# Kernel optimization log

Hardware: AMD Instinct MI355X
Metric: run time of the kernel (lower is better)

Reference implementation:

```python
import jax, jax.numpy as jnp
import numpy as np

N_NODES = 50000
NUM_FEA = 213
HID, IN_HEAD = 16, 12
OUT_DIM, OUT_HEAD = 8, 8
NEG_SLOPE = 0.2


def gat_conv(x, W, att_src, att_dst, bias, src, dst, H, C):
    # x: [N, F] -> h: [N, H, C]
    N = x.shape[0]
    h = (x @ W).reshape(N, H, C)
    a_s = jnp.sum(h * att_src, axis=-1)  # [N, H]
    a_d = jnp.sum(h * att_dst, axis=-1)  # [N, H]
    e = jax.nn.leaky_relu(a_s[src] + a_d[dst], NEG_SLOPE)  # [E, H]
    # segment softmax over incoming edges of each dst node
    m = jax.ops.segment_max(e, dst, num_segments=N)
    ex = jnp.exp(e - m[dst])
    denom = jax.ops.segment_sum(ex, dst, num_segments=N)
    alpha = ex / denom[dst]  # [E, H]
    out = jax.ops.segment_sum(h[src] * alpha[:, :, None], dst, num_segments=N)
    return out.reshape(N, H * C) + bias


def setup_inputs() -> dict:
    key = jax.random.key(0)
    ks = jax.random.split(key, 16)
    E = 800000
    P = 16384
    features = jax.random.normal(ks[0], (N_NODES, NUM_FEA), dtype=jnp.float32)
    edge_index = jax.random.randint(ks[1], (2, E), 0, N_NODES, dtype=jnp.int32)
    node1_index = jax.random.randint(ks[2], (P,), 0, N_NODES, dtype=jnp.int32)
    node2_index = jax.random.randint(ks[3], (P,), 0, N_NODES, dtype=jnp.int32)
    s1 = 1.0 / np.sqrt(NUM_FEA)
    s2 = 1.0 / np.sqrt(HID * IN_HEAD)
    s3 = 1.0 / np.sqrt(OUT_DIM * OUT_HEAD * 2)
    params = {
        'W1': jax.random.normal(ks[4], (NUM_FEA, IN_HEAD * HID), jnp.float32) * s1,
        'att_src1': jax.random.normal(ks[5], (IN_HEAD, HID), jnp.float32) * s1,
        'att_dst1': jax.random.normal(ks[6], (IN_HEAD, HID), jnp.float32) * s1,
        'b1': jnp.zeros((IN_HEAD * HID,), jnp.float32),
        'W2': jax.random.normal(ks[7], (IN_HEAD * HID, OUT_HEAD * OUT_DIM), jnp.float32) * s2,
        'att_src2': jax.random.normal(ks[8], (OUT_HEAD, OUT_DIM), jnp.float32) * s2,
        'att_dst2': jax.random.normal(ks[9], (OUT_HEAD, OUT_DIM), jnp.float32) * s2,
        'b2': jnp.zeros((OUT_HEAD * OUT_DIM,), jnp.float32),
        'linW': jax.random.normal(ks[10], (OUT_DIM * OUT_HEAD * 2, 2), jnp.float32) * s3,
        'linb': jnp.zeros((2,), jnp.float32),
    }
    return dict(features=features, edge_index=edge_index,
                node1_index=node1_index, node2_index=node2_index, **params)


def reference(features, edge_index, node1_index, node2_index,
              W1, att_src1, att_dst1, b1, W2, att_src2, att_dst2, b2, linW, linb):
    # eval mode: dropout(p=0.8) is identity
    N = features.shape[0]
    self_loops = jnp.arange(N, dtype=edge_index.dtype)
    src = jnp.concatenate([edge_index[0], self_loops])
    dst = jnp.concatenate([edge_index[1], self_loops])
    x = gat_conv(features, W1, att_src1, att_dst1, b1, src, dst, IN_HEAD, HID)
    x = jax.nn.elu(x)
    x = gat_conv(x, W2, att_src2, att_dst2, b2, src, dst, OUT_HEAD, OUT_DIM)
    x = jax.nn.elu(x)
    pair = jnp.concatenate([x[node1_index], x[node2_index]], axis=1)
    y_pred = jax.nn.sigmoid(pair @ linW + linb)
    return (y_pred, x)
```

## Files before the change

kernel.cpp:

```cpp
#include <hip/hip_runtime.h>
#include <hip/hip_bf16.h>

#define HID1 16
#define NHEAD1 12
#define F1 (HID1*NHEAD1)
#define HID2 8
#define NHEAD2 8
#define F2 (HID2*NHEAD2)
#define NUM_FEA 213
#define NEG_SLOPE 0.2f
#define KP 224
#define KP2 192
#define LDK 40
#define MR1 64
#define MR2 64
#define NC1 224
#define NW2R 80
#define SLOTS 56
#define BINS 256
#define NPB 196
#define CAP 4096
#define FILLB 256
#define EPT 13

typedef __attribute__((ext_vector_type(8))) __bf16 bf16x8;
typedef __attribute__((ext_vector_type(4))) float floatx4;
typedef __attribute__((ext_vector_type(2))) float floatx2;
typedef float floatx4u __attribute__((ext_vector_type(4), aligned(4)));
typedef unsigned short ushort_t;

static __device__ __forceinline__ unsigned short f2bf(float f) {
    unsigned u = __float_as_uint(f);
    unsigned r = (u + 0x7fffu + ((u >> 16) & 1u)) >> 16;
    return (unsigned short)r;
}
static __device__ __forceinline__ float lrelu(float e) {
    return e > 0.f ? e : NEG_SLOPE * e;
}
static __device__ __forceinline__ float elu(float v) {
    return v > 0.f ? v : (__expf(v) - 1.f);
}


__global__ __launch_bounds__(256) void prep_kernel(
        const float* __restrict__ W1, const float* __restrict__ as1w,
        const float* __restrict__ ad1w, ushort_t* __restrict__ Wt1,
        const float* __restrict__ W2, const float* __restrict__ as2w,
        const float* __restrict__ ad2w, ushort_t* __restrict__ Wt2,
        const int* __restrict__ ei, int* __restrict__ binctr,
        unsigned* __restrict__ binbuf, int E, int Etot, int nwb) {
    int b = (int)blockIdx.x;
    int tid = threadIdx.x;
    if (b >= nwb) {
        __shared__ int hist[BINS];
        __shared__ int cur[BINS];
        int fb = b - nwb;
        if (tid < BINS) hist[tid] = 0;
        __syncthreads();
        unsigned stash[EPT];
        int base_e = fb * 256 + tid;
#pragma unroll
        for (int i = 0; i < EPT; i++) {
            int e = base_e + i * (FILLB * 256);
            unsigned pk = 0xffffffffu;
            if (e < Etot) {
                int s, d;
                if (e < E) { s = ei[e]; d = ei[E + e]; } else { s = e - E; d = s; }
                pk = (unsigned)s | ((unsigned)d << 16);
                atomicAdd(&hist[(unsigned)d / NPB], 1);
            }
            stash[i] = pk;
        }
        __syncthreads();
        if (tid < BINS) cur[tid] = atomicAdd(&binctr[tid], hist[tid]);
        __syncthreads();
#pragma unroll
        for (int i = 0; i < EPT; i++) {
            unsigned pk = stash[i];
            if (pk != 0xffffffffu) {
                int d = (int)(pk >> 16);
                int bin = (int)((unsigned)d / NPB);
                int dl = d - bin * NPB;
                int r = atomicAdd(&cur[bin], 1);
                if (r < CAP)
                    binbuf[(long)bin * CAP + r] = (pk & 0xffffu) | ((unsigned)dl << 16);
            }
        }
        return;
    }
    int j = b * 256 + tid;
    if (j < NC1 * KP) {
        int n = j / KP, k = j - n * KP;
        float v = 0.f;
        if (k < NUM_FEA) {
            if (n < 192) {
                v = W1[(long)k * F1 + n];
            } else if (n < 204) {
                int hd = n - 192;
                for (int c = 0; c < HID1; c++)
                    v += W1[(long)k * F1 + hd * HID1 + c] * as1w[hd * HID1 + c];
            } else if (n < 216) {
                int hd = n - 204;
                for (int c = 0; c < HID1; c++)
                    v += W1[(long)k * F1 + hd * HID1 + c] * ad1w[hd * HID1 + c];
            }
        }
        Wt1[j] = f2bf(v);
    } else {
        int j2 = j - NC1 * KP;
        if (j2 < NW2R * KP2) {
            int n = j2 / KP2, k = j2 - n * KP2;
            float v;
            if (n < 64) {
                v = W2[(long)k * F2 + n];
            } else if (n < 72) {
                int hd = n - 64;
                v = 0.f;
                for (int c = 0; c < HID2; c++)
                    v += W2[(long)k * F2 + hd * HID2 + c] * as2w[hd * HID2 + c];
            } else {
                int hd = n - 72;
                v = 0.f;
                for (int c = 0; c < HID2; c++)
                    v += W2[(long)k * F2 + hd * HID2 + c] * ad2w[hd * HID2 + c];
            }
            Wt2[j2] = f2bf(v);
        }
    }
}


static __device__ __forceinline__ void stageA(ushort_t* dst, const float* xp,
                                              bool ok, int col) {
    union { int4 q; ushort_t u[8]; } pk;
    if (ok && col + 8 <= NUM_FEA) {
        floatx4u a = *(const floatx4u*)(xp + col);
        floatx4u c = *(const floatx4u*)(xp + col + 4);
#pragma unroll
        for (int j = 0; j < 4; j++) { pk.u[j] = f2bf(a[j]); pk.u[4 + j] = f2bf(c[j]); }
    } else {
#pragma unroll
        for (int j = 0; j < 8; j++) {
            float v = (ok && col + j < NUM_FEA) ? xp[col + j] : 0.f;
            pk.u[j] = f2bf(v);
        }
    }
    *(int4*)dst = pk.q;
}

__global__ __launch_bounds__(256) void gemm1_bs_kernel(
        const float* __restrict__ X, const ushort_t* __restrict__ Wt,
        ushort_t* __restrict__ Hout, float* __restrict__ as_, float* __restrict__ ad_,
        const unsigned* __restrict__ binbuf, const int* __restrict__ binctr,
        ushort_t* __restrict__ esrcp, int* __restrict__ cnt,
        int N, int nblk_gemm) {
    __shared__ ushort_t As[MR1 * LDK];
    __shared__ ushort_t Bs[NC1 * LDK];
    __shared__ int lcnt[NPB];
    int tid = threadIdx.x;
    if ((int)blockIdx.x >= nblk_gemm) {
        int b = (int)blockIdx.x - nblk_gemm;
        if (tid < NPB) lcnt[tid] = 0;
        __syncthreads();
        int cntb = binctr[b];
        if (cntb > CAP) cntb = CAP;
        const unsigned* seg = binbuf + (long)b * CAP;
        for (int t = tid; t < cntb; t += 256) {
            unsigned u = seg[t];
            int s = (int)(u & 0xffffu);
            int dl = (int)(u >> 16);
            int slot = atomicAdd(&lcnt[dl], 1);
            if (slot < SLOTS)
                esrcp[(long)(b * NPB + dl) * SLOTS + slot] = (ushort_t)s;
        }
        __syncthreads();
        int d = b * NPB + tid;
        if (tid < NPB && d < N) cnt[d] = lcnt[tid];
        return;
    }
    int wave = tid >> 6, lane = tid & 63;
    int q = lane >> 4, l16 = lane & 15;
    int wm = (wave >> 1) * 32;
    int wn = (wave & 1) * 112;
    long row0 = (long)blockIdx.x * MR1;

    int r0 = tid >> 2, ksl = (tid & 3) * 8;
    long gr0 = row0 + r0;
    bool ok0 = gr0 < N;
    const float* xp0 = X + gr0 * NUM_FEA;
    ushort_t* lds0 = &As[r0 * LDK + ksl];

    floatx4 acc[2][7] = {};

    for (int k0 = 0; k0 < KP; k0 += 32) {
        stageA(lds0, xp0, ok0, k0 + ksl);
#pragma unroll
        for (int p = 0; p < 4; p++) {
            int idx = p * 256 + tid;
            if (idx < NC1 * 4) {
                int r = idx >> 2, ks = (idx & 3) * 8;
                *(int4*)&Bs[r * LDK + ks] = *(const int4*)&Wt[(long)r * KP + k0 + ks];
            }
        }
        __syncthreads();
        bf16x8 af[2], bfr[7];
#pragma unroll
        for (int rt = 0; rt < 2; rt++)
            af[rt] = *(const bf16x8*)&As[(wm + rt * 16 + l16) * LDK + q * 8];
#pragma unroll
        for (int ct = 0; ct < 7; ct++)
            bfr[ct] = *(const bf16x8*)&Bs[(wn + ct * 16 + l16) * LDK + q * 8];
#pragma unroll
        for (int rt = 0; rt < 2; rt++)
#pragma unroll
            for (int ct = 0; ct < 7; ct++)
                acc[rt][ct] = __builtin_amdgcn_mfma_f32_16x16x32_bf16(af[rt], bfr[ct], acc[rt][ct], 0, 0, 0);
        __syncthreads();
    }
#pragma unroll
    for (int rt = 0; rt < 2; rt++) {
#pragma unroll
        for (int r = 0; r < 4; r++) {
            long grow = row0 + wm + rt * 16 + q * 4 + r;
            if (grow < N) {
#pragma unroll
                for (int ct = 0; ct < 7; ct++) {
                    int col = wn + ct * 16 + l16;
                    float v = acc[rt][ct][r];
                    if (col < 192)      Hout[grow * F1 + col] = f2bf(v);
                    else if (col < 204) as_[grow * NHEAD1 + col - 192] = v;
                    else if (col < 216) ad_[grow * NHEAD1 + col - 204] = v;
                }
            }
        }
    }
}


__global__ __launch_bounds__(256) void gemm2_mfma(const ushort_t* __restrict__ Xbf,
                                                  const ushort_t* __restrict__ Wt,
                                                  ushort_t* __restrict__ Hout,
                                                  float* __restrict__ as_,
                                                  float* __restrict__ ad_, int N) {
    __shared__ ushort_t As[MR2 * LDK];
    __shared__ ushort_t Bs[96 * LDK];
    int tid = threadIdx.x;
    int wave = tid >> 6, lane = tid & 63;
    int q = lane >> 4, l16 = lane & 15;
    int wm = (wave >> 1) * 32;
    int wn = (wave & 1) * 48;
    long row0 = (long)blockIdx.x * MR2;

    int r0 = tid >> 2, ksl = (tid & 3) * 8;

    floatx4 acc[2][3] = {};

    for (int k0 = 0; k0 < KP2; k0 += 32) {
        *(int4*)&As[r0 * LDK + ksl] = *(const int4*)&Xbf[(row0 + r0) * KP2 + k0 + ksl];
#pragma unroll
        for (int p = 0; p < 2; p++) {
            int idx = p * 256 + tid;
            if (idx < 96 * 4) {
                int r = idx >> 2, ks = (idx & 3) * 8;
                int4 z = {0, 0, 0, 0};
                *(int4*)&Bs[r * LDK + ks] = (r < NW2R) ? *(const int4*)&Wt[(long)r * KP2 + k0 + ks] : z;
            }
        }
        __syncthreads();
        bf16x8 af[2], bfr[3];
#pragma unroll
        for (int rt = 0; rt < 2; rt++)
            af[rt] = *(const bf16x8*)&As[(wm + rt * 16 + l16) * LDK + q * 8];
#pragma unroll
        for (int ct = 0; ct < 3; ct++)
            bfr[ct] = *(const bf16x8*)&Bs[(wn + ct * 16 + l16) * LDK + q * 8];
#pragma unroll
        for (int rt = 0; rt < 2; rt++)
#pragma unroll
            for (int ct = 0; ct < 3; ct++)
                acc[rt][ct] = __builtin_amdgcn_mfma_f32_16x16x32_bf16(af[rt], bfr[ct], acc[rt][ct], 0, 0, 0);
        __syncthreads();
    }
#pragma unroll
    for (int rt = 0; rt < 2; rt++) {
#pragma unroll
        for (int r = 0; r < 4; r++) {
            long grow = row0 + wm + rt * 16 + q * 4 + r;
            if (grow < N) {
#pragma unroll
                for (int ct = 0; ct < 3; ct++) {
                    int col = wn + ct * 16 + l16;
                    float v = acc[rt][ct][r];
                    if (col < 64)      Hout[grow * F2 + col] = f2bf(v);
                    else if (col < 72) as_[grow * NHEAD2 + col - 64] = v;
                    else if (col < 80) ad_[grow * NHEAD2 + col - 72] = v;
                }
            }
        }
    }
}


__global__ __launch_bounds__(256) void gather1_kernel(const int* __restrict__ cnt,
                                                      const ushort_t* __restrict__ esrcp,
                                                      const float* __restrict__ as_,
                                                      const float* __restrict__ ad_,
                                                      const ushort_t* __restrict__ h,
                                                      const float* __restrict__ bias,
                                                      ushort_t* __restrict__ xout, int N) {
    int d = blockIdx.x * 4 + (threadIdx.x >> 6);
    if (d >= N) return;
    int l = threadIdx.x & 63;
    int jc = l < 48 ? l : 47;
    int hj = jc >> 2;
    int e0 = l / 12, h0 = l - e0 * 12;
    int l64 = l + 64;
    int e1 = l64 / 12, h1 = l64 - e1 * 12;
    int deg = cnt[d]; if (deg > SLOTS) deg = SLOTS;
    int sfull = (int)esrcp[d * SLOTS + (l < SLOTS - 1 ? l : SLOTS - 1)];
    float adv0 = ad_[d * NHEAD1 + h0];
    float adv1 = ad_[d * NHEAD1 + h1];
    float4 b4 = ((const float4*)bias)[jc];
    const char* hcol = (const char*)(h + 4 * jc);

    floatx2 a01 = {0.f, 0.f}, a23 = {0.f, 0.f};
    float accd = 0.f;

    for (int p0 = 0; p0 < deg; p0 += 8) {
        int s_e[8];
#pragma unroll
        for (int i = 0; i < 8; i++) s_e[i] = __shfl(sfull, p0 + i, 64);
        uint2 g[8];
#pragma unroll
        for (int i = 0; i < 8; i++) {
            unsigned off = (unsigned)s_e[i] * (unsigned)(F1 * 2);
            g[i] = *(const uint2*)(hcol + off);
        }
        int sq0 = __shfl(sfull, p0 + e0, 64);
        int sq1 = __shfl(sfull, p0 + e1, 64);
        float a0v = as_[sq0 * NHEAD1 + h0];
        float a1v = as_[sq1 * NHEAD1 + h1];
        float w0 = (p0 + e0 < deg) ? __expf(lrelu(a0v + adv0)) : 0.f;
        float w1 = (e1 < 8 && p0 + e1 < deg) ? __expf(lrelu(a1v + adv1)) : 0.f;
#pragma unroll
        for (int i = 0; i < 8; i++) {
            float wi;
            if (i <= 4) {
                wi = __shfl(w0, i * 12 + hj, 64);
            } else if (i == 5) {
                float wa = __shfl(w0, 60 + hj, 64);
                int srcb = hj >= 4 ? hj - 4 : 0;
                float wb = __shfl(w1, srcb, 64);
                wi = (hj < 4) ? wa : wb;
            } else {
                wi = __shfl(w1, i * 12 + hj - 64, 64);
            }
            unsigned x = g[i].x, y = g[i].y;
            floatx2 h01, h23, w2;
            h01.x = __uint_as_float(x << 16);
            h01.y = __uint_as_float(x & 0xffff0000u);
            h23.x = __uint_as_float(y << 16);
            h23.y = __uint_as_float(y & 0xffff0000u);
            w2.x = wi; w2.y = wi;
            a01 += w2 * h01;
            a23 += w2 * h23;
            accd += wi;
        }
    }
    if (l < 48) {
        float inv = __builtin_amdgcn_rcpf(accd);
        float v0 = elu(a01.x * inv + b4.x);
        float v1 = elu(a01.y * inv + b4.y);
        float v2 = elu(a23.x * inv + b4.z);
        float v3 = elu(a23.y * inv + b4.w);
        uint2 outp;
        outp.x = (unsigned)f2bf(v0) | ((unsigned)f2bf(v1) << 16);
        outp.y = (unsigned)f2bf(v2) | ((unsigned)f2bf(v3) << 16);
        *(uint2*)(xout + (long)d * F1 + 4 * l) = outp;
    }
}


__global__ __launch_bounds__(256) void gather2_kernel(const int* __restrict__ cnt,
                                                      const ushort_t* __restrict__ esrcp,
                                                      const float* __restrict__ as_,
                                                      const float* __restrict__ ad_,
                                                      const ushort_t* __restrict__ h,
                                                      const float* __restrict__ bias,
                                                      float* __restrict__ xout, int N) {
    int d = blockIdx.x * 4 + (threadIdx.x >> 6);
    if (d >= N) return;
    int l = threadIdx.x & 63;
    int cg = l & 15;
    int hj = cg >> 1;
    int e_lo = l >> 4;
    int ie0 = l >> 3, hq = l & 7;
    int ie1 = 8 + ie0;
    int deg = cnt[d]; if (deg > SLOTS) deg = SLOTS;
    int sfull = (int)esrcp[d * SLOTS + (l < SLOTS - 1 ? l : SLOTS - 1)];
    float advq = ad_[d * NHEAD2 + hq];
    const char* hcol = (const char*)(h + 4 * cg);

    floatx2 a01 = {0.f, 0.f}, a23 = {0.f, 0.f};
    float accd = 0.f;

    for (int p0 = 0; p0 < deg; p0 += 16) {
        int se[4];
#pragma unroll
        for (int k = 0; k < 4; k++) se[k] = __shfl(sfull, p0 + e_lo + 4 * k, 64);
        uint2 g[4];
#pragma unroll
        for (int k = 0; k < 4; k++) {
            unsigned off = (unsigned)se[k] * (unsigned)(F2 * 2);
            g[k] = *(const uint2*)(hcol + off);
        }
        int sq0 = __shfl(sfull, p0 + ie0, 64);
        int sq1 = __shfl(sfull, p0 + ie1, 64);
        float a0v = as_[sq0 * NHEAD2 + hq];
        float a1v = as_[sq1 * NHEAD2 + hq];
        float w0d = (p0 + ie0 < deg) ? __expf(lrelu(a0v + advq)) : 0.f;
        float w1d = (p0 + ie1 < deg) ? __expf(lrelu(a1v + advq)) : 0.f;
#pragma unroll
        for (int k = 0; k < 4; k++) {
            int i = e_lo + 4 * k;
            float wk = (k < 2) ? __shfl(w0d, i * 8 + hj, 64)
                               : __shfl(w1d, i * 8 + hj - 64, 64);
            unsigned x = g[k].x, y = g[k].y;
            floatx2 h01, h23, w2;
            h01.x = __uint_as_float(x << 16);
            h01.y = __uint_as_float(x & 0xffff0000u);
            h23.x = __uint_as_float(y << 16);
            h23.y = __uint_as_float(y & 0xffff0000u);
            w2.x = wk; w2.y = wk;
            a01 += w2 * h01;
            a23 += w2 * h23;
            accd += wk;
        }
    }
    a01.x += __shfl_xor(a01.x, 16, 64); a01.x += __shfl_xor(a01.x, 32, 64);
    a01.y += __shfl_xor(a01.y, 16, 64); a01.y += __shfl_xor(a01.y, 32, 64);
    a23.x += __shfl_xor(a23.x, 16, 64); a23.x += __shfl_xor(a23.x, 32, 64);
    a23.y += __shfl_xor(a23.y, 16, 64); a23.y += __shfl_xor(a23.y, 32, 64);
    accd  += __shfl_xor(accd, 16, 64);  accd  += __shfl_xor(accd, 32, 64);
    if (l < 16) {
        float4 b4 = ((const float4*)bias)[cg];
        float inv = __builtin_amdgcn_rcpf(accd);
        float4 outp;
        outp.x = elu(a01.x * inv + b4.x);
        outp.y = elu(a01.y * inv + b4.y);
        outp.z = elu(a23.x * inv + b4.z);
        outp.w = elu(a23.y * inv + b4.w);
        *(float4*)(xout + (long)d * F2 + 4 * cg) = outp;
    }
}


__global__ void pair_kernel(const float* __restrict__ x, const int* __restrict__ n1,
                            const int* __restrict__ n2, const float* __restrict__ linW,
                            const float* __restrict__ linb, float* __restrict__ y, int P) {
    int idx = blockIdx.x * blockDim.x + threadIdx.x;
    if (idx >= P) return;
    const float4* xa = (const float4*)(x + (long)n1[idx] * F2);
    const float4* xb = (const float4*)(x + (long)n2[idx] * F2);
    float a0 = linb[0], a1 = linb[1];
#pragma unroll
    for (int k4 = 0; k4 < F2 / 4; k4++) {
        float4 v = xa[k4];
        int k = k4 * 4;
        a0 += v.x * linW[2 * k] + v.y * linW[2 * (k + 1)] + v.z * linW[2 * (k + 2)] + v.w * linW[2 * (k + 3)];
        a1 += v.x * linW[2 * k + 1] + v.y * linW[2 * (k + 1) + 1] + v.z * linW[2 * (k + 2) + 1] + v.w * linW[2 * (k + 3) + 1];
    }
#pragma unroll
    for (int k4 = 0; k4 < F2 / 4; k4++) {
        float4 v = xb[k4];
        int k = F2 + k4 * 4;
        a0 += v.x * linW[2 * k] + v.y * linW[2 * (k + 1)] + v.z * linW[2 * (k + 2)] + v.w * linW[2 * (k + 3)];
        a1 += v.x * linW[2 * k + 1] + v.y * linW[2 * (k + 1) + 1] + v.z * linW[2 * (k + 2) + 1] + v.w * linW[2 * (k + 3) + 1];
    }
    y[2 * idx]     = 1.f / (1.f + __expf(-a0));
    y[2 * idx + 1] = 1.f / (1.f + __expf(-a1));
}


extern "C" void kernel_launch(void* const* d_in, const int* in_sizes, int n_in,
                              void* d_out, int out_size, void* d_ws, size_t ws_size,
                              hipStream_t stream) {
    const float* features = (const float*)d_in[0];
    const int*   ei       = (const int*)d_in[1];
    const int*   n1       = (const int*)d_in[2];
    const int*   n2       = (const int*)d_in[3];
    const float* W1       = (const float*)d_in[4];
    const float* att_s1   = (const float*)d_in[5];
    const float* att_d1   = (const float*)d_in[6];
    const float* b1       = (const float*)d_in[7];
    const float* W2       = (const float*)d_in[8];
    const float* att_s2   = (const float*)d_in[9];
    const float* att_d2   = (const float*)d_in[10];
    const float* b2       = (const float*)d_in[11];
    const float* linW     = (const float*)d_in[12];
    const float* linb     = (const float*)d_in[13];

    const int N = in_sizes[0] / NUM_FEA;
    const int E = in_sizes[1] / 2;
    const int P = in_sizes[2];
    const int Etot = E + N;

    const int nblk1 = (N + MR1 - 1) / MR1;
    const int nblk2 = (N + MR2 - 1) / MR2;
    const int nwb = (NC1 * KP + NW2R * KP2 + 255) / 256;

    float* ws = (float*)d_ws;
    long o = 0;
    float* h1r  = ws + o; o += (long)N * F1 / 2;
    float* x1r  = ws + o; o += (long)N * F1 / 2;
    float* as1  = ws + o; o += (long)N * NHEAD1;
    float* ad1  = ws + o; o += (long)N * NHEAD1;
    float* h2r  = ws + o; o += (long)N * F2 / 2;
    float* as2  = ws + o; o += (long)N * NHEAD2;
    float* ad2  = ws + o; o += (long)N * NHEAD2;
    float* w1r  = ws + o; o += ((long)NC1 * KP + 1) / 2;
    float* w2r  = ws + o; o += ((long)NW2R * KP2 + 1) / 2;
    float* esr  = ws + o; o += ((long)N * SLOTS + 1) / 2;
    unsigned* binbuf = (unsigned*)(ws + o); o += (long)BINS * CAP;
    int* binctr = (int*)(ws + o); o += BINS;
    int* cnt  = (int*)(ws + o); o += N;

    ushort_t* h1b   = (ushort_t*)h1r;
    ushort_t* x1bf  = (ushort_t*)x1r;
    ushort_t* h2b   = (ushort_t*)h2r;
    ushort_t* Wt1   = (ushort_t*)w1r;
    ushort_t* Wt2   = (ushort_t*)w2r;
    ushort_t* esrcp = (ushort_t*)esr;

    float* y_out = (float*)d_out;
    float* x_out = (float*)d_out + (long)2 * P;

    hipMemsetAsync(binctr, 0, (size_t)BINS * sizeof(int), stream);

    prep_kernel<<<nwb + FILLB, 256, 0, stream>>>(
        W1, att_s1, att_d1, Wt1, W2, att_s2, att_d2, Wt2,
        ei, binctr, binbuf, E, Etot, nwb);

    gemm1_bs_kernel<<<nblk1 + BINS, 256, 0, stream>>>(
        features, Wt1, h1b, as1, ad1, binbuf, binctr, esrcp, cnt, N, nblk1);

    gather1_kernel<<<(N + 3) / 4, 256, 0, stream>>>(cnt, esrcp, as1, ad1, h1b, b1, x1bf, N);

    gemm2_mfma<<<nblk2, 256, 0, stream>>>(x1bf, Wt2, h2b, as2, ad2, N);
    gather2_kernel<<<(N + 3) / 4, 256, 0, stream>>>(cnt, esrcp, as2, ad2, h2b, b2, x_out, N);

    pair_kernel<<<(P + 255) / 256, 256, 0, stream>>>(x_out, n1, n2, linW, linb, y_out, P);
}
```

Measured before the change: 252.0 us.

## Move edge binning fill into GEMM1 launch and split bin sort into own kernel

The edge binning fill stage moves out of the weight-prep kernel and runs as extra blocks alongside the GEMM1 blocks. The per-bin local sort, which previously shared the GEMM1 launch, now runs in its own small kernel afterwards. The goal is to overlap the memory-bound edge fill with the compute-bound GEMM and shorten the prep kernel. The cost is one extra kernel launch and larger shared memory use in the GEMM1 kernel for the histogram arrays, which may reduce occupancy.

```diff
diff --git a/kernel.cpp b/kernel.cpp
--- a/kernel.cpp
+++ b/kernel.cpp
@@ -42,53 +42,12 @@
 }
 
 
-__global__ __launch_bounds__(256) void prep_kernel(
+__global__ __launch_bounds__(256) void wprep_kernel(
         const float* __restrict__ W1, const float* __restrict__ as1w,
         const float* __restrict__ ad1w, ushort_t* __restrict__ Wt1,
         const float* __restrict__ W2, const float* __restrict__ as2w,
-        const float* __restrict__ ad2w, ushort_t* __restrict__ Wt2,
-        const int* __restrict__ ei, int* __restrict__ binctr,
-        unsigned* __restrict__ binbuf, int E, int Etot, int nwb) {
-    int b = (int)blockIdx.x;
-    int tid = threadIdx.x;
-    if (b >= nwb) {
-        __shared__ int hist[BINS];
-        __shared__ int cur[BINS];
-        int fb = b - nwb;
-        if (tid < BINS) hist[tid] = 0;
-        __syncthreads();
-        unsigned stash[EPT];
-        int base_e = fb * 256 + tid;
-#pragma unroll
-        for (int i = 0; i < EPT; i++) {
-            int e = base_e + i * (FILLB * 256);
-            unsigned pk = 0xffffffffu;
-            if (e < Etot) {
-                int s, d;
-                if (e < E) { s = ei[e]; d = ei[E + e]; } else { s = e - E; d = s; }
-                pk = (unsigned)s | ((unsigned)d << 16);
-                atomicAdd(&hist[(unsigned)d / NPB], 1);
-            }
-            stash[i] = pk;
-        }
-        __syncthreads();
-        if (tid < BINS) cur[tid] = atomicAdd(&binctr[tid], hist[tid]);
-        __syncthreads();
-#pragma unroll
-        for (int i = 0; i < EPT; i++) {
-            unsigned pk = stash[i];
-            if (pk != 0xffffffffu) {
-                int d = (int)(pk >> 16);
-                int bin = (int)((unsigned)d / NPB);
-                int dl = d - bin * NPB;
-                int r = atomicAdd(&cur[bin], 1);
-                if (r < CAP)
-                    binbuf[(long)bin * CAP + r] = (pk & 0xffffu) | ((unsigned)dl << 16);
-            }
-        }
-        return;
-    }
-    int j = b * 256 + tid;
+        const float* __restrict__ ad2w, ushort_t* __restrict__ Wt2) {
+    int j = blockIdx.x * 256 + threadIdx.x;
     if (j < NC1 * KP) {
         int n = j / KP, k = j - n * KP;
         float v = 0.f;
@@ -148,34 +107,50 @@
     *(int4*)dst = pk.q;
 }
 
-__global__ __launch_bounds__(256) void gemm1_bs_kernel(
+__global__ __launch_bounds__(256) void gemm1_fill_kernel(
         const float* __restrict__ X, const ushort_t* __restrict__ Wt,
         ushort_t* __restrict__ Hout, float* __restrict__ as_, float* __restrict__ ad_,
-        const unsigned* __restrict__ binbuf, const int* __restrict__ binctr,
-        ushort_t* __restrict__ esrcp, int* __restrict__ cnt,
+        const int* __restrict__ ei, int* __restrict__ binctr,
+        unsigned* __restrict__ binbuf, int E, int Etot,
         int N, int nblk_gemm) {
     __shared__ ushort_t As[MR1 * LDK];
     __shared__ ushort_t Bs[NC1 * LDK];
-    __shared__ int lcnt[NPB];
+    __shared__ int hist[BINS];
+    __shared__ int cur[BINS];
     int tid = threadIdx.x;
     if ((int)blockIdx.x >= nblk_gemm) {
-        int b = (int)blockIdx.x - nblk_gemm;
-        if (tid < NPB) lcnt[tid] = 0;
-        __syncthreads();
-        int cntb = binctr[b];
-        if (cntb > CAP) cntb = CAP;
-        const unsigned* seg = binbuf + (long)b * CAP;
-        for (int t = tid; t < cntb; t += 256) {
-            unsigned u = seg[t];
-            int s = (int)(u & 0xffffu);
-            int dl = (int)(u >> 16);
-            int slot = atomicAdd(&lcnt[dl], 1);
-            if (slot < SLOTS)
-                esrcp[(long)(b * NPB + dl) * SLOTS + slot] = (ushort_t)s;
-        }
-        __syncthreads();
-        int d = b * NPB + tid;
-        if (tid < NPB && d < N) cnt[d] = lcnt[tid];
+        int fb = (int)blockIdx.x - nblk_gemm;
+        if (tid < BINS) hist[tid] = 0;
+        __syncthreads();
+        unsigned stash[EPT];
+        int base_e = fb * 256 + tid;
+#pragma unroll
+        for (int i = 0; i < EPT; i++) {
+            int e = base_e + i * (FILLB * 256);
+            unsigned pk = 0xffffffffu;
+            if (e < Etot) {
+                int s, d;
+                if (e < E) { s = ei[e]; d = ei[E + e]; } else { s = e - E; d = s; }
+                pk = (unsigned)s | ((unsigned)d << 16);
+                atomicAdd(&hist[(unsigned)d / NPB], 1);
+            }
+            stash[i] = pk;
+        }
+        __syncthreads();
+        if (tid < BINS) cur[tid] = atomicAdd(&binctr[tid], hist[tid]);
+        __syncthreads();
+#pragma unroll
+        for (int i = 0; i < EPT; i++) {
+            unsigned pk = stash[i];
+            if (pk != 0xffffffffu) {
+                int d = (int)(pk >> 16);
+                int bin = (int)((unsigned)d / NPB);
+                int dl = d - bin * NPB;
+                int r = atomicAdd(&cur[bin], 1);
+                if (r < CAP)
+                    binbuf[(long)bin * CAP + r] = (pk & 0xffffu) | ((unsigned)dl << 16);
+            }
+        }
         return;
     }
     int wave = tid >> 6, lane = tid & 63;
@@ -234,6 +209,30 @@
             }
         }
     }
+}
+
+
+__global__ __launch_bounds__(256) void binsort_kernel(
+        const unsigned* __restrict__ binbuf, const int* __restrict__ binctr,
+        ushort_t* __restrict__ esrcp, int* __restrict__ cnt, int N) {
+    __shared__ int lcnt[NPB];
+    int b = blockIdx.x, tid = threadIdx.x;
+    if (tid < NPB) lcnt[tid] = 0;
+    __syncthreads();
+    int cntb = binctr[b];
+    if (cntb > CAP) cntb = CAP;
+    const unsigned* seg = binbuf + (long)b * CAP;
+    for (int t = tid; t < cntb; t += 256) {
+        unsigned u = seg[t];
+        int s = (int)(u & 0xffffu);
+        int dl = (int)(u >> 16);
+        int slot = atomicAdd(&lcnt[dl], 1);
+        if (slot < SLOTS)
+            esrcp[(long)(b * NPB + dl) * SLOTS + slot] = (ushort_t)s;
+    }
+    __syncthreads();
+    int d = b * NPB + tid;
+    if (tid < NPB && d < N) cnt[d] = lcnt[tid];
 }
 
 
@@ -537,12 +536,13 @@
 
     hipMemsetAsync(binctr, 0, (size_t)BINS * sizeof(int), stream);
 
-    prep_kernel<<<nwb + FILLB, 256, 0, stream>>>(
-        W1, att_s1, att_d1, Wt1, W2, att_s2, att_d2, Wt2,
-        ei, binctr, binbuf, E, Etot, nwb);
-
-    gemm1_bs_kernel<<<nblk1 + BINS, 256, 0, stream>>>(
-        features, Wt1, h1b, as1, ad1, binbuf, binctr, esrcp, cnt, N, nblk1);
+    wprep_kernel<<<nwb, 256, 0, stream>>>(W1, att_s1, att_d1, Wt1,
+                                          W2, att_s2, att_d2, Wt2);
+
+    gemm1_fill_kernel<<<nblk1 + FILLB, 256, 0, stream>>>(
+        features, Wt1, h1b, as1, ad1, ei, binctr, binbuf, E, Etot, N, nblk1);
+
+    binsort_kernel<<<BINS, 256, 0, stream>>>(binbuf, binctr, esrcp, cnt, N);
 
     gather1_kernel<<<(N + 3) / 4, 256, 0, stream>>>(cnt, esrcp, as1, ad1, h1b, b1, x1bf, N);
 
```

Result: no change. 249.1 us (-1.2%).
